# Optimization experiments

Measured on AMD Instinct MI355X. Metric: run time of the kernel, lower is better.

The kernel has to match this reference:

```python
import jax, jax.numpy as jnp
import numpy as np

N = 100000   # nodes
E = 640000   # edges
DIN = 128
DOUT = 128
BN_EPS = 1e-5


def setup_inputs() -> dict:
    key = jax.random.key(0)
    k = jax.random.split(key, 6)
    x = jax.random.normal(k[0], (N, DIN), dtype=jnp.float32)
    edge_index = jax.random.randint(k[1], (2, E), 0, N, dtype=jnp.int64)
    # MLP params: Linear(DIN,DOUT) -> BatchNorm1d(DOUT) -> ReLU -> Linear(DOUT,DOUT)
    s1 = 1.0 / np.sqrt(DIN)
    s2 = 1.0 / np.sqrt(DOUT)
    W1 = jax.random.uniform(k[2], (DIN, DOUT), jnp.float32, -s1, s1)
    b1 = jax.random.uniform(k[3], (DOUT,), jnp.float32, -s1, s1)
    gamma = jnp.ones((DOUT,), jnp.float32)
    beta = jnp.zeros((DOUT,), jnp.float32)
    W2 = jax.random.uniform(k[4], (DOUT, DOUT), jnp.float32, -s2, s2)
    b2 = jax.random.uniform(k[5], (DOUT,), jnp.float32, -s2, s2)
    eps = jnp.zeros((), jnp.float32)  # train_eps=True, init 0.0
    return {"x": x, "edge_index": edge_index, "W1": W1, "b1": b1,
            "gamma": gamma, "beta": beta, "W2": W2, "b2": b2, "eps": eps}


def reference(x, edge_index, W1, b1, gamma, beta, W2, b2, eps):
    src = edge_index[0]
    dst = edge_index[1]
    # GIN sum aggregation: gather source features, scatter-add to target nodes
    agg = jax.ops.segment_sum(x[src], dst, num_segments=N)  # [N, DIN]
    h = agg + (1.0 + eps) * x  # eps-weighted residual combine
    # MLP: Linear -> BatchNorm1d (training stats, biased var) -> ReLU -> Linear
    h = h @ W1 + b1  # [N, DOUT]
    mu = jnp.mean(h, axis=0)
    var = jnp.mean((h - mu) ** 2, axis=0)
    h = (h - mu) * jax.lax.rsqrt(var + BN_EPS) * gamma + beta
    h = jnp.maximum(h, 0.0)
    return h @ W2 + b2
```

## Files before the change

kernel.cpp:

```cpp
#include <hip/hip_runtime.h>

#define N_NODES 100000
#define DIM     128
#define NEDGE   640000
#define BN_EPS  1e-5f

#define PB_CNT  2500
#define PB_X    6250
#define PB_W    64

#define NSLOT   32
#define NBUCKET 64
#define T_TILES 4
#define GGRID   1563
#define AGRID   6250

typedef __bf16 bf16x8 __attribute__((ext_vector_type(8)));
typedef float  f32x4  __attribute__((ext_vector_type(4)));
typedef unsigned short u16x8 __attribute__((ext_vector_type(8)));

__device__ __forceinline__ unsigned short f2b(float f) {
    unsigned u = __builtin_bit_cast(unsigned, f);
    u += 0x7fffu + ((u >> 16) & 1u);
    return (unsigned short)(u >> 16);
}
__device__ __forceinline__ float b2f(unsigned short b) {
    return __builtin_bit_cast(float, ((unsigned)b) << 16);
}

__global__ __launch_bounds__(256) void k_prep(const float* __restrict__ x,
                                              const float* __restrict__ W1,
                                              const float* __restrict__ W2,
                                              const int* __restrict__ ei,
                                              unsigned short* __restrict__ xb,
                                              unsigned short* __restrict__ Wt1,
                                              unsigned short* __restrict__ Wt2,
                                              unsigned* __restrict__ cnt,
                                              int* __restrict__ slots) {
    const int b = blockIdx.x;
    const int t = threadIdx.x;
    if (b < PB_CNT) {
        int e = b * 256 + t;
        int src = ei[e];
        int dst = ei[NEDGE + e];
        unsigned r0 = (unsigned)e & 3u;
        #pragma unroll
        for (int a = 0; a < 4; ++a) {
            unsigned rr = (r0 + a) & 3u;
            unsigned old = atomicAdd(&cnt[dst], 1u << (8u * rr));
            unsigned rk = (old >> (8u * rr)) & 255u;
            if (rk < 8u) {
                slots[dst * NSLOT + rr * 8 + rk] = src;
                break;
            }
        }
    } else if (b < PB_CNT + PB_X) {
        size_t base = ((size_t)(b - PB_CNT) * 256 + t) * 8;
        float4 v0 = *(const float4*)(x + base);
        float4 v1 = *(const float4*)(x + base + 4);
        u16x8 o;
        o[0] = f2b(v0.x); o[1] = f2b(v0.y); o[2] = f2b(v0.z); o[3] = f2b(v0.w);
        o[4] = f2b(v1.x); o[5] = f2b(v1.y); o[6] = f2b(v1.z); o[7] = f2b(v1.w);
        *(u16x8*)(xb + base) = o;
    } else if (b < PB_CNT + PB_X + PB_W) {
        int idx = (b - PB_CNT - PB_X) * 256 + t;
        int k = idx >> 7, n = idx & 127;
        Wt1[n * 128 + k] = f2b(W1[idx]);
    } else {
        int idx = (b - PB_CNT - PB_X - PB_W) * 256 + t;
        int k = idx >> 7, n = idx & 127;
        Wt2[n * 128 + k] = f2b(W2[idx]);
    }
}

__global__ __launch_bounds__(256) void k_agg1(const unsigned short* __restrict__ xb,
                                              const unsigned* __restrict__ cnt,
                                              const int* __restrict__ slots,
                                              const float* __restrict__ epsp,
                                              const unsigned short* __restrict__ Wt,
                                              const float* __restrict__ b1,
                                              unsigned short* __restrict__ hB,
                                              float* __restrict__ buckets) {
    __shared__ __align__(16) unsigned short At[16 * 136];
    __shared__ __align__(16) unsigned short stage[4][512];
    const int t = threadIdx.x;
    const int w = t >> 6;
    const int lane = t & 63;
    const int n15 = lane & 15;
    const int quad = lane >> 4;
    const int c8 = n15 * 8;
    const int gbase = lane & 48;

    const int row0 = blockIdx.x * 16;
    const int node = row0 + w * 4 + quad;

    int4 Bfr[2][4];
    const unsigned short* wp = Wt + (w * 32 + n15) * 128 + quad * 8;
    #pragma unroll
    for (int c = 0; c < 2; ++c)
        #pragma unroll
        for (int ks = 0; ks < 4; ++ks)
            Bfr[c][ks] = *(const int4*)(wp + c * 16 * 128 + ks * 32);
    float bias[2] = { b1[w * 32 + n15], b1[w * 32 + 16 + n15] };
    const float scale = 1.0f + epsp[0];

    const unsigned cw = cnt[node];
    const int s_lo = slots[node * NSLOT + n15];
    const int s_hi = slots[node * NSLOT + 16 + n15];
    float acc[8];
    {
        u16x8 v = *(const u16x8*)(xb + (size_t)node * 128 + c8);
        #pragma unroll
        for (int j = 0; j < 8; ++j) acc[j] = scale * b2f(v[j]);
    }
    unsigned m = 0;
    #pragma unroll
    for (int r = 0; r < 4; ++r) {
        unsigned d = (cw >> (8 * r)) & 255u;
        d = d > 8u ? 8u : d;
        m |= ((1u << d) - 1u) << (8 * r);
    }
    const int navail = __popc(m);
    unsigned mm = m;
    int pk = 0;
    for (int done = 0; done < navail; done += 8) {
        int4 va[8];
        #pragma unroll
        for (int k = 0; k < 8; ++k) {
            if (mm) { pk = (int)__builtin_ctz(mm); mm &= (mm - 1); }
            int vlo = __shfl(s_lo, gbase + (pk & 15));
            int vhi = __shfl(s_hi, gbase + (pk & 15));
            int srck = (pk & 16) ? vhi : vlo;
            va[k] = *(const int4*)(xb + (size_t)srck * 128 + c8);
        }
        const int rem = navail - done;
        #pragma unroll
        for (int k = 0; k < 8; ++k) {
            if (k < rem) {
                u16x8 v = __builtin_bit_cast(u16x8, va[k]);
                #pragma unroll
                for (int j = 0; j < 8; ++j) acc[j] += b2f(v[j]);
            }
        }
    }
    {
        u16x8 o;
        #pragma unroll
        for (int j = 0; j < 8; ++j) o[j] = f2b(acc[j]);
        *(u16x8*)(At + (w * 4 + quad) * 136 + c8) = o;
    }
    __syncthreads();

    f32x4 accm[2] = {};
    #pragma unroll
    for (int ks = 0; ks < 4; ++ks) {
        int4 araw = *(const int4*)(At + n15 * 136 + ks * 32 + quad * 8);
        bf16x8 af = __builtin_bit_cast(bf16x8, araw);
        #pragma unroll
        for (int c = 0; c < 2; ++c)
            accm[c] = __builtin_amdgcn_mfma_f32_16x16x32_bf16(
                af, __builtin_bit_cast(bf16x8, Bfr[c][ks]), accm[c], 0, 0, 0);
    }
    float s[2] = {0.f, 0.f}, q[2] = {0.f, 0.f};
    unsigned short* st = stage[w];
    #pragma unroll
    for (int c = 0; c < 2; ++c)
        #pragma unroll
        for (int r = 0; r < 4; ++r) {
            float v = accm[c][r] + bias[c];
            s[c] += v; q[c] += v * v;
            st[(quad * 4 + r) * 32 + c * 16 + n15] = f2b(v);
        }
    {
        int so = lane * 8;
        int r = so >> 5, cc = so & 31;
        *(int4*)(hB + (size_t)(row0 + r) * 128 + w * 32 + cc) = *(const int4*)(st + so);
    }

    #pragma unroll
    for (int c = 0; c < 2; ++c) {
        s[c] += __shfl_down(s[c], 32); q[c] += __shfl_down(q[c], 32);
        s[c] += __shfl_down(s[c], 16); q[c] += __shfl_down(q[c], 16);
    }
    if (quad == 0) {
        float* bk = buckets + (blockIdx.x & (NBUCKET - 1)) * 256;
        atomicAdd(&bk[w * 32 + n15], s[0]);
        atomicAdd(&bk[w * 32 + 16 + n15], s[1]);
        atomicAdd(&bk[128 + w * 32 + n15], q[0]);
        atomicAdd(&bk[128 + w * 32 + 16 + n15], q[1]);
    }
}

__global__ void k_finalize(const float* __restrict__ gamma,
                           const float* __restrict__ beta,
                           const float* __restrict__ buckets,
                           float* __restrict__ aff) {
    int c = threadIdx.x;
    if (c < DIM) {
        float s = 0.f, q = 0.f;
        #pragma unroll 8
        for (int b = 0; b < NBUCKET; ++b) {
            s += buckets[b * 256 + c];
            q += buckets[b * 256 + 128 + c];
        }
        float mu  = s * (1.0f / N_NODES);
        float var = q * (1.0f / N_NODES) - mu * mu;
        float a = gamma[c] * rsqrtf(var + BN_EPS);
        aff[c] = a;
        aff[DIM + c] = beta[c] - mu * a;
    }
}

__global__ __launch_bounds__(256) void k_gemm2(const unsigned short* __restrict__ hb,
                                               const unsigned short* __restrict__ Wt2,
                                               const float* __restrict__ aff,
                                               const float* __restrict__ b2,
                                               float* __restrict__ out) {
    __shared__ __align__(16) unsigned short Asb[2][16 * 136];
    __shared__ __align__(16) float stage[4][512];
    const int t = threadIdx.x;
    const int w = t >> 6;
    const int lane = t & 63;
    const int n15 = lane & 15;
    const int quad = lane >> 4;
    const int kb = w * 32 + quad * 8;

    int4 Bfr[2][4];
    const unsigned short* wp = Wt2 + (w * 32 + n15) * 128 + quad * 8;
    #pragma unroll
    for (int c = 0; c < 2; ++c)
        #pragma unroll
        for (int ks = 0; ks < 4; ++ks)
            Bfr[c][ks] = *(const int4*)(wp + c * 16 * 128 + ks * 32);

    float akr[8], bkr[8];
    *(float4*)(akr)     = *(const float4*)(aff + kb);
    *(float4*)(akr + 4) = *(const float4*)(aff + kb + 4);
    *(float4*)(bkr)     = *(const float4*)(aff + 128 + kb);
    *(float4*)(bkr + 4) = *(const float4*)(aff + 128 + kb + 4);
    float bias[2] = { b2[w * 32 + n15], b2[w * 32 + 16 + n15] };

    const int tile0 = blockIdx.x * T_TILES;
    int4 gr;
    {
        int r0 = tile0 * 16;
        if (r0 < N_NODES)
            gr = *(const int4*)(hb + (size_t)(r0 + n15) * 128 + kb);
    }
    float* st = stage[w];

    #pragma unroll
    for (int i = 0; i < T_TILES; ++i) {
        const int row0 = (tile0 + i) * 16;
        const bool valid = row0 < N_NODES;
        unsigned short* al = Asb[i & 1];
        if (valid) {
            u16x8 ar = __builtin_bit_cast(u16x8, gr);
            u16x8 pr;
            #pragma unroll
            for (int j = 0; j < 8; ++j)
                pr[j] = f2b(fmaxf(fmaf(b2f(ar[j]), akr[j], bkr[j]), 0.f));
            *(int4*)(al + n15 * 136 + kb) = __builtin_bit_cast(int4, pr);
        }
        if (i + 1 < T_TILES) {
            int rn = (tile0 + i + 1) * 16;
            if (rn < N_NODES)
                gr = *(const int4*)(hb + (size_t)(rn + n15) * 128 + kb);
        }
        __syncthreads();
        if (valid) {
            f32x4 acc[2] = {};
            #pragma unroll
            for (int ks = 0; ks < 4; ++ks) {
                int4 araw = *(const int4*)(al + n15 * 136 + ks * 32 + quad * 8);
                bf16x8 af = __builtin_bit_cast(bf16x8, araw);
                #pragma unroll
                for (int c = 0; c < 2; ++c)
                    acc[c] = __builtin_amdgcn_mfma_f32_16x16x32_bf16(
                        af, __builtin_bit_cast(bf16x8, Bfr[c][ks]), acc[c], 0, 0, 0);
            }
            #pragma unroll
            for (int c = 0; c < 2; ++c)
                #pragma unroll
                for (int r = 0; r < 4; ++r)
                    st[(quad * 4 + r) * 32 + c * 16 + n15] = acc[c][r] + bias[c];
            #pragma unroll
            for (int p = 0; p < 2; ++p) {
                int fo = p * 256 + lane * 4;
                int r = fo >> 5, cc = fo & 31;
                *(float4*)(out + (size_t)(row0 + r) * 128 + w * 32 + cc) =
                    *(const float4*)(st + fo);
            }
        }
    }
}

extern "C" void kernel_launch(void* const* d_in, const int* in_sizes, int n_in,
                              void* d_out, int out_size, void* d_ws, size_t ws_size,
                              hipStream_t stream) {
    const float* x     = (const float*)d_in[0];
    const int*   ei    = (const int*)d_in[1];
    const float* W1    = (const float*)d_in[2];
    const float* b1    = (const float*)d_in[3];
    const float* gamma = (const float*)d_in[4];
    const float* beta  = (const float*)d_in[5];
    const float* W2    = (const float*)d_in[6];
    const float* b2    = (const float*)d_in[7];
    const float* eps   = (const float*)d_in[8];
    float* out = (float*)d_out;

    float* buckets      = (float*)d_ws;
    unsigned* cnt       = (unsigned*)(buckets + NBUCKET * 256);
    float* aff          = (float*)(cnt + N_NODES);
    unsigned short* hB  = (unsigned short*)(aff + 256);
    unsigned short* xb  = hB + (size_t)N_NODES * DIM;
    unsigned short* Wt1 = xb + (size_t)N_NODES * DIM;
    unsigned short* Wt2 = Wt1 + 16384;
    int* slots          = (int*)(Wt2 + 16384);

    hipMemsetAsync(buckets, 0,
                   NBUCKET * 256 * sizeof(float) + N_NODES * sizeof(unsigned), stream);

    k_prep<<<PB_CNT + PB_X + 2 * PB_W, 256, 0, stream>>>(x, W1, W2, ei, xb, Wt1, Wt2,
                                                         cnt, slots);
    k_agg1<<<AGRID, 256, 0, stream>>>(xb, cnt, slots, eps, Wt1, b1, hB, buckets);
    k_finalize<<<1, 128, 0, stream>>>(gamma, beta, buckets, aff);
    k_gemm2<<<GGRID, 256, 0, stream>>>(hB, Wt2, aff, b2, out);
}
```

Baseline: 206.7 us.

## Fuse BN finalize into gemm2 and split per-node counters into four words

Removes the single-block finalize kernel by having every gemm2 block reduce the bucketed BN statistics itself into shared memory before use. The per-node slot counters change from one packed word with byte fields to four separate 32-bit counters, so the atomics and the mask build in the aggregation kernel become simpler. This saves a kernel launch and the serial dependency, but every block redundantly reads the 64-bucket statistics array, and the counter array and its memset grow fourfold.

```diff
diff --git a/kernel.cpp b/kernel.cpp
--- a/kernel.cpp
+++ b/kernel.cpp
@@ -43,16 +43,15 @@
         int e = b * 256 + t;
         int src = ei[e];
         int dst = ei[NEDGE + e];
-        unsigned r0 = (unsigned)e & 3u;
+        unsigned r = (unsigned)e & 3u;
         #pragma unroll
         for (int a = 0; a < 4; ++a) {
-            unsigned rr = (r0 + a) & 3u;
-            unsigned old = atomicAdd(&cnt[dst], 1u << (8u * rr));
-            unsigned rk = (old >> (8u * rr)) & 255u;
+            unsigned rk = atomicAdd(&cnt[dst * 4 + r], 1u);
             if (rk < 8u) {
-                slots[dst * NSLOT + rr * 8 + rk] = src;
+                slots[dst * NSLOT + r * 8 + rk] = src;
                 break;
             }
+            r = (r + 1) & 3u;
         }
     } else if (b < PB_CNT + PB_X) {
         size_t base = ((size_t)(b - PB_CNT) * 256 + t) * 8;
@@ -104,7 +103,7 @@
     float bias[2] = { b1[w * 32 + n15], b1[w * 32 + 16 + n15] };
     const float scale = 1.0f + epsp[0];
 
-    const unsigned cw = cnt[node];
+    const uint4 cw = *(const uint4*)(cnt + node * 4);
     const int s_lo = slots[node * NSLOT + n15];
     const int s_hi = slots[node * NSLOT + 16 + n15];
     float acc[8];
@@ -113,12 +112,14 @@
         #pragma unroll
         for (int j = 0; j < 8; ++j) acc[j] = scale * b2f(v[j]);
     }
-    unsigned m = 0;
-    #pragma unroll
-    for (int r = 0; r < 4; ++r) {
-        unsigned d = (cw >> (8 * r)) & 255u;
-        d = d > 8u ? 8u : d;
-        m |= ((1u << d) - 1u) << (8 * r);
+    unsigned m;
+    {
+        unsigned d0 = cw.x > 8u ? 8u : cw.x;
+        unsigned d1 = cw.y > 8u ? 8u : cw.y;
+        unsigned d2 = cw.z > 8u ? 8u : cw.z;
+        unsigned d3 = cw.w > 8u ? 8u : cw.w;
+        m = ((1u << d0) - 1u) | (((1u << d1) - 1u) << 8) |
+            (((1u << d2) - 1u) << 16) | (((1u << d3) - 1u) << 24);
     }
     const int navail = __popc(m);
     unsigned mm = m;
@@ -191,33 +192,16 @@
     }
 }
 
-__global__ void k_finalize(const float* __restrict__ gamma,
-                           const float* __restrict__ beta,
-                           const float* __restrict__ buckets,
-                           float* __restrict__ aff) {
-    int c = threadIdx.x;
-    if (c < DIM) {
-        float s = 0.f, q = 0.f;
-        #pragma unroll 8
-        for (int b = 0; b < NBUCKET; ++b) {
-            s += buckets[b * 256 + c];
-            q += buckets[b * 256 + 128 + c];
-        }
-        float mu  = s * (1.0f / N_NODES);
-        float var = q * (1.0f / N_NODES) - mu * mu;
-        float a = gamma[c] * rsqrtf(var + BN_EPS);
-        aff[c] = a;
-        aff[DIM + c] = beta[c] - mu * a;
-    }
-}
-
 __global__ __launch_bounds__(256) void k_gemm2(const unsigned short* __restrict__ hb,
                                                const unsigned short* __restrict__ Wt2,
-                                               const float* __restrict__ aff,
+                                               const float* __restrict__ buckets,
+                                               const float* __restrict__ gamma,
+                                               const float* __restrict__ beta,
                                                const float* __restrict__ b2,
                                                float* __restrict__ out) {
     __shared__ __align__(16) unsigned short Asb[2][16 * 136];
     __shared__ __align__(16) float stage[4][512];
+    __shared__ __align__(16) float aff_s[256];
     const int t = threadIdx.x;
     const int w = t >> 6;
     const int lane = t & 63;
@@ -225,21 +209,6 @@
     const int quad = lane >> 4;
     const int kb = w * 32 + quad * 8;
 
-    int4 Bfr[2][4];
-    const unsigned short* wp = Wt2 + (w * 32 + n15) * 128 + quad * 8;
-    #pragma unroll
-    for (int c = 0; c < 2; ++c)
-        #pragma unroll
-        for (int ks = 0; ks < 4; ++ks)
-            Bfr[c][ks] = *(const int4*)(wp + c * 16 * 128 + ks * 32);
-
-    float akr[8], bkr[8];
-    *(float4*)(akr)     = *(const float4*)(aff + kb);
-    *(float4*)(akr + 4) = *(const float4*)(aff + kb + 4);
-    *(float4*)(bkr)     = *(const float4*)(aff + 128 + kb);
-    *(float4*)(bkr + 4) = *(const float4*)(aff + 128 + kb + 4);
-    float bias[2] = { b2[w * 32 + n15], b2[w * 32 + 16 + n15] };
-
     const int tile0 = blockIdx.x * T_TILES;
     int4 gr;
     {
@@ -247,6 +216,37 @@
         if (r0 < N_NODES)
             gr = *(const int4*)(hb + (size_t)(r0 + n15) * 128 + kb);
     }
+
+    int4 Bfr[2][4];
+    const unsigned short* wp = Wt2 + (w * 32 + n15) * 128 + quad * 8;
+    #pragma unroll
+    for (int c = 0; c < 2; ++c)
+        #pragma unroll
+        for (int ks = 0; ks < 4; ++ks)
+            Bfr[c][ks] = *(const int4*)(wp + c * 16 * 128 + ks * 32);
+    float bias[2] = { b2[w * 32 + n15], b2[w * 32 + 16 + n15] };
+
+    if (t < 128) {
+        float s = 0.f, q = 0.f;
+        #pragma unroll 8
+        for (int b = 0; b < NBUCKET; ++b) {
+            s += buckets[b * 256 + t];
+            q += buckets[b * 256 + 128 + t];
+        }
+        float mu  = s * (1.0f / N_NODES);
+        float var = q * (1.0f / N_NODES) - mu * mu;
+        float a = gamma[t] * rsqrtf(var + BN_EPS);
+        aff_s[t] = a;
+        aff_s[128 + t] = beta[t] - mu * a;
+    }
+    __syncthreads();
+
+    float akr[8], bkr[8];
+    *(float4*)(akr)     = *(const float4*)(aff_s + kb);
+    *(float4*)(akr + 4) = *(const float4*)(aff_s + kb + 4);
+    *(float4*)(bkr)     = *(const float4*)(aff_s + 128 + kb);
+    *(float4*)(bkr + 4) = *(const float4*)(aff_s + 128 + kb + 4);
+
     float* st = stage[w];
 
     #pragma unroll
@@ -311,19 +311,18 @@
 
     float* buckets      = (float*)d_ws;
     unsigned* cnt       = (unsigned*)(buckets + NBUCKET * 256);
-    float* aff          = (float*)(cnt + N_NODES);
-    unsigned short* hB  = (unsigned short*)(aff + 256);
+    unsigned short* hB  = (unsigned short*)(cnt + 4 * N_NODES);
     unsigned short* xb  = hB + (size_t)N_NODES * DIM;
     unsigned short* Wt1 = xb + (size_t)N_NODES * DIM;
     unsigned short* Wt2 = Wt1 + 16384;
     int* slots          = (int*)(Wt2 + 16384);
 
     hipMemsetAsync(buckets, 0,
-                   NBUCKET * 256 * sizeof(float) + N_NODES * sizeof(unsigned), stream);
+                   NBUCKET * 256 * sizeof(float) + 4 * N_NODES * sizeof(unsigned),
+                   stream);
 
     k_prep<<<PB_CNT + PB_X + 2 * PB_W, 256, 0, stream>>>(x, W1, W2, ei, xb, Wt1, Wt2,
                                                          cnt, slots);
     k_agg1<<<AGRID, 256, 0, stream>>>(xb, cnt, slots, eps, Wt1, b1, hB, buckets);
-    k_finalize<<<1, 128, 0, stream>>>(gamma, beta, buckets, aff);
-    k_gemm2<<<GGRID, 256, 0, stream>>>(hB, Wt2, aff, b2, out);
-}
+    k_gemm2<<<GGRID, 256, 0, stream>>>(hB, Wt2, buckets, gamma, beta, b2, out);
+}
```

New measurement: 208.9 us. No clear change (+1.1%).

## Replace packed-counter slot table with CAS-based open-addressed slots and simplify gemm2 loads

Applied to the files above, without the earlier changes.

The adjacency build drops the per-node packed 8-bit counters. Each edge now claims a free slot in a 32-entry per-node table by linear-probing atomicCAS against a 0xFFFFFFFF sentinel, and the aggregation kernel finds occupied slots with a wave ballot instead of decoding counts. This removes the cnt array and its reads, but adds a 12.8 MB memset of the slot table to 0xFF plus CAS probing. In gemm2, the A tile is now loaded with a row-per-quad layout read directly inside each tile iteration, replacing the software prefetch of the next tile.

```diff
diff --git a/kernel.cpp b/kernel.cpp
--- a/kernel.cpp
+++ b/kernel.cpp
@@ -35,24 +35,20 @@
                                               unsigned short* __restrict__ xb,
                                               unsigned short* __restrict__ Wt1,
                                               unsigned short* __restrict__ Wt2,
-                                              unsigned* __restrict__ cnt,
-                                              int* __restrict__ slots) {
+                                              unsigned* __restrict__ slots) {
     const int b = blockIdx.x;
     const int t = threadIdx.x;
     if (b < PB_CNT) {
         int e = b * 256 + t;
-        int src = ei[e];
+        unsigned src = (unsigned)ei[e];
         int dst = ei[NEDGE + e];
-        unsigned r0 = (unsigned)e & 3u;
-        #pragma unroll
-        for (int a = 0; a < 4; ++a) {
-            unsigned rr = (r0 + a) & 3u;
-            unsigned old = atomicAdd(&cnt[dst], 1u << (8u * rr));
-            unsigned rk = (old >> (8u * rr)) & 255u;
-            if (rk < 8u) {
-                slots[dst * NSLOT + rr * 8 + rk] = src;
-                break;
-            }
+        unsigned* sp = slots + (size_t)dst * NSLOT;
+        unsigned h = (unsigned)e;
+        #pragma unroll 1
+        for (int i = 0; i < NSLOT; ++i) {
+            unsigned s = (h + (unsigned)i) & (NSLOT - 1);
+            unsigned old = atomicCAS(&sp[s], 0xFFFFFFFFu, src);
+            if (old == 0xFFFFFFFFu) break;
         }
     } else if (b < PB_CNT + PB_X) {
         size_t base = ((size_t)(b - PB_CNT) * 256 + t) * 8;
@@ -74,8 +70,7 @@
 }
 
 __global__ __launch_bounds__(256) void k_agg1(const unsigned short* __restrict__ xb,
-                                              const unsigned* __restrict__ cnt,
-                                              const int* __restrict__ slots,
+                                              const unsigned* __restrict__ slots,
                                               const float* __restrict__ epsp,
                                               const unsigned short* __restrict__ Wt,
                                               const float* __restrict__ b1,
@@ -104,22 +99,18 @@
     float bias[2] = { b1[w * 32 + n15], b1[w * 32 + 16 + n15] };
     const float scale = 1.0f + epsp[0];
 
-    const unsigned cw = cnt[node];
-    const int s_lo = slots[node * NSLOT + n15];
-    const int s_hi = slots[node * NSLOT + 16 + n15];
+    const unsigned s_lo = slots[(size_t)node * NSLOT + n15];
+    const unsigned s_hi = slots[(size_t)node * NSLOT + 16 + n15];
     float acc[8];
     {
         u16x8 v = *(const u16x8*)(xb + (size_t)node * 128 + c8);
         #pragma unroll
         for (int j = 0; j < 8; ++j) acc[j] = scale * b2f(v[j]);
     }
-    unsigned m = 0;
-    #pragma unroll
-    for (int r = 0; r < 4; ++r) {
-        unsigned d = (cw >> (8 * r)) & 255u;
-        d = d > 8u ? 8u : d;
-        m |= ((1u << d) - 1u) << (8 * r);
-    }
+    unsigned long long blo = __ballot(s_lo != 0xFFFFFFFFu);
+    unsigned long long bhi = __ballot(s_hi != 0xFFFFFFFFu);
+    unsigned m = (unsigned)((blo >> gbase) & 0xFFFFull) |
+                 ((unsigned)((bhi >> gbase) & 0xFFFFull) << 16);
     const int navail = __popc(m);
     unsigned mm = m;
     int pk = 0;
@@ -128,9 +119,9 @@
         #pragma unroll
         for (int k = 0; k < 8; ++k) {
             if (mm) { pk = (int)__builtin_ctz(mm); mm &= (mm - 1); }
-            int vlo = __shfl(s_lo, gbase + (pk & 15));
-            int vhi = __shfl(s_hi, gbase + (pk & 15));
-            int srck = (pk & 16) ? vhi : vlo;
+            unsigned vlo = __shfl(s_lo, gbase + (pk & 15));
+            unsigned vhi = __shfl(s_hi, gbase + (pk & 15));
+            unsigned srck = (pk & 16) ? vhi : vlo;
             va[k] = *(const int4*)(xb + (size_t)srck * 128 + c8);
         }
         const int rem = navail - done;
@@ -223,7 +214,8 @@
     const int lane = t & 63;
     const int n15 = lane & 15;
     const int quad = lane >> 4;
-    const int kb = w * 32 + quad * 8;
+    const int c8 = n15 * 8;
+    const int lrow = w * 4 + quad;
 
     int4 Bfr[2][4];
     const unsigned short* wp = Wt2 + (w * 32 + n15) * 128 + quad * 8;
@@ -234,19 +226,13 @@
             Bfr[c][ks] = *(const int4*)(wp + c * 16 * 128 + ks * 32);
 
     float akr[8], bkr[8];
-    *(float4*)(akr)     = *(const float4*)(aff + kb);
-    *(float4*)(akr + 4) = *(const float4*)(aff + kb + 4);
-    *(float4*)(bkr)     = *(const float4*)(aff + 128 + kb);
-    *(float4*)(bkr + 4) = *(const float4*)(aff + 128 + kb + 4);
+    *(float4*)(akr)     = *(const float4*)(aff + c8);
+    *(float4*)(akr + 4) = *(const float4*)(aff + c8 + 4);
+    *(float4*)(bkr)     = *(const float4*)(aff + 128 + c8);
+    *(float4*)(bkr + 4) = *(const float4*)(aff + 128 + c8 + 4);
     float bias[2] = { b2[w * 32 + n15], b2[w * 32 + 16 + n15] };
 
     const int tile0 = blockIdx.x * T_TILES;
-    int4 gr;
-    {
-        int r0 = tile0 * 16;
-        if (r0 < N_NODES)
-            gr = *(const int4*)(hb + (size_t)(r0 + n15) * 128 + kb);
-    }
     float* st = stage[w];
 
     #pragma unroll
@@ -255,17 +241,13 @@
         const bool valid = row0 < N_NODES;
         unsigned short* al = Asb[i & 1];
         if (valid) {
-            u16x8 ar = __builtin_bit_cast(u16x8, gr);
+            int4 graw = *(const int4*)(hb + (size_t)(row0 + lrow) * 128 + c8);
+            u16x8 ar = __builtin_bit_cast(u16x8, graw);
             u16x8 pr;
             #pragma unroll
             for (int j = 0; j < 8; ++j)
                 pr[j] = f2b(fmaxf(fmaf(b2f(ar[j]), akr[j], bkr[j]), 0.f));
-            *(int4*)(al + n15 * 136 + kb) = __builtin_bit_cast(int4, pr);
-        }
-        if (i + 1 < T_TILES) {
-            int rn = (tile0 + i + 1) * 16;
-            if (rn < N_NODES)
-                gr = *(const int4*)(hb + (size_t)(rn + n15) * 128 + kb);
+            *(int4*)(al + lrow * 136 + c8) = __builtin_bit_cast(int4, pr);
         }
         __syncthreads();
         if (valid) {
@@ -310,20 +292,19 @@
     float* out = (float*)d_out;
 
     float* buckets      = (float*)d_ws;
-    unsigned* cnt       = (unsigned*)(buckets + NBUCKET * 256);
-    float* aff          = (float*)(cnt + N_NODES);
+    float* aff          = (float*)(buckets + NBUCKET * 256);
     unsigned short* hB  = (unsigned short*)(aff + 256);
     unsigned short* xb  = hB + (size_t)N_NODES * DIM;
     unsigned short* Wt1 = xb + (size_t)N_NODES * DIM;
     unsigned short* Wt2 = Wt1 + 16384;
-    int* slots          = (int*)(Wt2 + 16384);
-
-    hipMemsetAsync(buckets, 0,
-                   NBUCKET * 256 * sizeof(float) + N_NODES * sizeof(unsigned), stream);
+    unsigned* slots     = (unsigned*)(Wt2 + 16384);
+
+    hipMemsetAsync(buckets, 0, NBUCKET * 256 * sizeof(float), stream);
+    hipMemsetAsync(slots, 0xFF, (size_t)N_NODES * NSLOT * sizeof(unsigned), stream);
 
     k_prep<<<PB_CNT + PB_X + 2 * PB_W, 256, 0, stream>>>(x, W1, W2, ei, xb, Wt1, Wt2,
-                                                         cnt, slots);
-    k_agg1<<<AGRID, 256, 0, stream>>>(xb, cnt, slots, eps, Wt1, b1, hB, buckets);
+                                                         slots);
+    k_agg1<<<AGRID, 256, 0, stream>>>(xb, slots, eps, Wt1, b1, hB, buckets);
     k_finalize<<<1, 128, 0, stream>>>(gamma, beta, buckets, aff);
     k_gemm2<<<GGRID, 256, 0, stream>>>(hB, Wt2, aff, b2, out);
 }
```

Result: no change. 206.3 us (-0.2%).
